# Optimization experiments

Hardware: AMD Instinct MI355X
Metric: run time of the kernel (lower is better)

## Reference

```python
import jax, jax.numpy as jnp
import numpy as np

NUM_ITERATIONS = 3
NUM_ROUTES = 6912  # 32*6*6*6


def _squash(t):
    # t: [..., O]; squash along last dim
    sq = jnp.sum(t * t, axis=-1, keepdims=True)
    return sq * t / ((1.0 + sq) * jnp.sqrt(sq))


def setup_inputs() -> dict:
    key = jax.random.key(0)
    k1, k2 = jax.random.split(key)
    B, R, I, C, O = 64, NUM_ROUTES, 8, 10, 16
    x = jax.random.normal(k1, (B, R, I), dtype=jnp.float32)
    route_weights = jax.random.normal(k2, (C, R, I, O), dtype=jnp.float32)
    return {"x": x, "route_weights": route_weights}


def reference(x, route_weights):
    # x: [B, R, I]; route_weights: [C, R, I, O]
    # priors = x[None,:,:,None,:] @ W[:,None,:,:,:] -> [C, B, R, 1, O]
    priors = jnp.einsum('bri,crio->cbro', x, route_weights)[:, :, :, None, :]
    logits = jnp.zeros_like(priors)  # [C, B, R, 1, O]
    outputs = None
    for i in range(NUM_ITERATIONS):
        # softmax over routes (dim=2), matching custom softmax(input, dim=2)
        probs = jax.nn.softmax(logits, axis=2)
        outputs = _squash(jnp.sum(probs * priors, axis=2, keepdims=True))  # [C,B,1,1,O]
        if i != NUM_ROUTES - 1:  # always true in original (num_routes >> iters)
            delta = jnp.sum(priors * outputs, axis=-1, keepdims=True)  # [C,B,R,1,1]
            logits = logits + delta
    return outputs
```

## Files before the change

kernel.cpp:

```cpp
#include <hip/hip_runtime.h>
#include <math.h>

#define BB 64
#define RR 6912
#define II 8
#define CC 10
#define OO 16
#define RPB2 96
#define NCH2 72
#define NG2 12
#define NBLK 720
#define NREP 9
#define MRG_PAD 20
#define WTILE_I4 (RPB2*16)
#define MRGF (4*64*MRG_PAD + 4*64)
#define ACCW (CC*NREP*BB*OO)
#define ZW   (CC*NREP*BB)
#define BARI (64 + NCH2*32 + NCH2*32)
#define ZWORDS (3*ACCW + 2*ZW + BARI)

typedef _Float16 h2 __attribute__((ext_vector_type(2)));
typedef _Float16 half8 __attribute__((ext_vector_type(8)));
typedef float f32x16 __attribute__((ext_vector_type(16)));
union HV { int4 v; h2 h[4]; half8 h8; };

__device__ __forceinline__ void addf(float* p, float v) {
    float old = __hip_atomic_fetch_add(p, v, __ATOMIC_RELAXED, __HIP_MEMORY_SCOPE_AGENT);
    asm volatile("" :: "v"(old));
}
__device__ __forceinline__ void addi(int* p) {
    int old = __hip_atomic_fetch_add(p, 1, __ATOMIC_RELAXED, __HIP_MEMORY_SCOPE_AGENT);
    asm volatile("" :: "v"(old));
}
__device__ __forceinline__ void xchi(int* p, int v) {
    int old = __hip_atomic_exchange(p, v, __ATOMIC_RELAXED, __HIP_MEMORY_SCOPE_AGENT);
    asm volatile("" :: "v"(old));
}
template <int SLP, int GUARD>
__device__ __forceinline__ void pollge(const int* p, int tgt) {
    int v = __hip_atomic_load(p, __ATOMIC_RELAXED, __HIP_MEMORY_SCOPE_AGENT);
    int g = 0;
    while (v < tgt && ++g < GUARD) {
        __builtin_amdgcn_s_sleep(SLP);
        v = __hip_atomic_load(p, __ATOMIC_RELAXED, __HIP_MEMORY_SCOPE_AGENT);
    }
}

__device__ __forceinline__ void gbar(int* bar, int chunk, int c, int phase) {
    __syncthreads();
    if (threadIdx.x == 0) {
        int* charr = bar + 64 + chunk * 32;
        int* chep  = bar + 64 + NCH2 * 32 + chunk * 32;
        addi(charr);
        if (c == 0) {
            pollge<4, (1 << 14)>(charr, 10 * phase);
            addi(bar + 0);
            if (chunk == 0) {
                pollge<8, (1 << 14)>(bar + 0, NCH2 * phase);
                xchi(bar + 32, phase);
            } else {
                pollge<32, (1 << 12)>(bar + 32, phase);
            }
            xchi(chep, phase);
        } else {
            pollge<8, (1 << 13)>(chep, phase);
        }
    }
    __syncthreads();
}

__global__ __launch_bounds__(256) void prep_kernel(
    const float* __restrict__ x, int4* __restrict__ xth4,
    const float4* __restrict__ w4, int4* __restrict__ wh4,
    float* __restrict__ zbase)
{
    __shared__ __align__(16) float4 lds4[64 * 34];
    const int t = threadIdx.x;
    const int bid = blockIdx.x;

    for (unsigned idx = (unsigned)bid * 256u + (unsigned)t; idx < (unsigned)ZWORDS;
         idx += 1512u * 256u)
        zbase[idx] = 0.f;

    if (bid < 432) {
        const int rblk = bid >> 2;
        const int bblk = bid & 3;
        const int r0 = rblk * 64, b0 = bblk * 16;
        {
            const int rl = t & 63;
            const int bl0 = t >> 6;
#pragma unroll
            for (int kb = 0; kb < 4; ++kb) {
                const int bl = kb * 4 + bl0;
                const float4* src = (const float4*)(x + ((size_t)(b0 + bl) * RR + (r0 + rl)) * II);
                lds4[rl * 34 + bl * 2 + 0] = src[0];
                lds4[rl * 34 + bl * 2 + 1] = src[1];
            }
        }
        __syncthreads();
        {
            const int bl = t & 15;
            const int rw0 = t >> 4;
#pragma unroll
            for (int kr = 0; kr < 4; ++kr) {
                const int rw = kr * 16 + rw0;
                float4 a = lds4[rw * 34 + bl * 2 + 0];
                float4 bq = lds4[rw * 34 + bl * 2 + 1];
                HV u;
                u.h[0] = h2{(_Float16)a.x,  (_Float16)a.y};
                u.h[1] = h2{(_Float16)a.z,  (_Float16)a.w};
                u.h[2] = h2{(_Float16)bq.x, (_Float16)bq.y};
                u.h[3] = h2{(_Float16)bq.z, (_Float16)bq.w};
                xth4[(size_t)(r0 + rw) * BB + (b0 + bl)] = u.v;
            }
        }
    } else {
        _Float16* wl = (_Float16*)lds4;
        const int wblk = bid - 432;
        const int rp = t >> 5;
        const int i  = (t >> 2) & 7;
        const int o0 = (t & 3) * 4;
#pragma unroll 1
        for (int sb = 0; sb < 8; ++sb) {
            const int blk8 = wblk * 8 + sb;
            const float4 v = w4[(size_t)blk8 * 256 + t];
            _Float16* wb = wl + (sb & 1) * 1024;
            wb[(rp * 16 + o0 + 0) * 8 + i] = (_Float16)v.x;
            wb[(rp * 16 + o0 + 1) * 8 + i] = (_Float16)v.y;
            wb[(rp * 16 + o0 + 2) * 8 + i] = (_Float16)v.z;
            wb[(rp * 16 + o0 + 3) * 8 + i] = (_Float16)v.w;
            __syncthreads();
            if (t < 128) wh4[(size_t)blk8 * 128 + t] = ((const int4*)wb)[t];
        }
    }
}

template <int MODE>
__device__ __forceinline__ void it_phase(
    const int4* __restrict__ xth4, const int4* wlds, float* mrg,
    const float* __restrict__ ov,
    float* __restrict__ acc, float* __restrict__ zacc,
    int c, int chunk, int t)
{
    const int wv = t >> 6;
    const int l = t & 63;
    const int b = l & 31;
    const int hi = l >> 5;
    const int aquad = (l >> 4) & 1;
    const bool aact = (aquad == hi);

    float accA[8], accB[8];
#pragma unroll
    for (int j = 0; j < 8; ++j) { accA[j] = 0.f; accB[j] = 0.f; }
    float ZA = 0.f, ZB = 0.f;

    float ovA[8], ovB[8];
    if (MODE != 0) {
        const float* pa = ov + ((size_t)c * BB + b) * OO + 4 * hi;
        const float* pb = ov + ((size_t)c * BB + 32 + b) * OO + 4 * hi;
        float4 a0 = *(const float4*)(pa);
        float4 a1 = *(const float4*)(pa + 8);
        float4 b0 = *(const float4*)(pb);
        float4 b1 = *(const float4*)(pb + 8);
        ovA[0]=a0.x; ovA[1]=a0.y; ovA[2]=a0.z; ovA[3]=a0.w;
        ovA[4]=a1.x; ovA[5]=a1.y; ovA[6]=a1.z; ovA[7]=a1.w;
        ovB[0]=b0.x; ovB[1]=b0.y; ovB[2]=b0.z; ovB[3]=b0.w;
        ovB[4]=b1.x; ovB[5]=b1.y; ovB[6]=b1.z; ovB[7]=b1.w;
    }

    const int rbase = chunk * RPB2 + wv * 24;

    f32x16 cA, cB, zf;
#pragma unroll
    for (int q = 0; q < 16; ++q) { cA[q] = 0.f; cB[q] = 0.f; zf[q] = 0.f; }

    HV xc0, xc1, xn0, xn1;
    xc0.v = xth4[(size_t)(rbase + hi) * BB + b];
    xc1.v = xth4[(size_t)(rbase + hi) * BB + 32 + b];
    xn0 = xc0; xn1 = xc1;

#pragma unroll 1
    for (int g = 0; g < NG2; ++g) {
        if (g + 1 < NG2) {
            const int rn = rbase + (g + 1) * 2 + hi;
            xn0.v = xth4[(size_t)rn * BB + b];
            xn1.v = xth4[(size_t)rn * BB + 32 + b];
        }
        const int rl0 = wv * 24 + g * 2;
        HV wq;
        wq.v = wlds[(rl0 + aquad) * 16 + (l & 15)];
        if (!aact) wq.v = make_int4(0, 0, 0, 0);

        if (MODE == 0) {
            cA = __builtin_amdgcn_mfma_f32_32x32x16_f16(wq.h8, xc0.h8, cA, 0, 0, 0);
            cB = __builtin_amdgcn_mfma_f32_32x32x16_f16(wq.h8, xc1.h8, cB, 0, 0, 0);
        } else {
            f32x16 p0 = __builtin_amdgcn_mfma_f32_32x32x16_f16(wq.h8, xc0.h8, zf, 0, 0, 0);
            f32x16 p1 = __builtin_amdgcn_mfma_f32_32x32x16_f16(wq.h8, xc1.h8, zf, 0, 0, 0);
            float dA0 = 0.f, dA1 = 0.f, dB0 = 0.f, dB1 = 0.f;
#pragma unroll
            for (int j = 0; j < 8; ++j) {
                dA0 = fmaf(p0[j],     ovA[j], dA0);
                dA1 = fmaf(p0[j + 8], ovA[j], dA1);
                dB0 = fmaf(p1[j],     ovB[j], dB0);
                dB1 = fmaf(p1[j + 8], ovB[j], dB1);
            }
            dA0 += __shfl_xor(dA0, 32);
            dA1 += __shfl_xor(dA1, 32);
            dB0 += __shfl_xor(dB0, 32);
            dB1 += __shfl_xor(dB1, 32);
            const float eA0 = __expf(dA0), eA1 = __expf(dA1);
            const float eB0 = __expf(dB0), eB1 = __expf(dB1);
            ZA += eA0 + eA1; ZB += eB0 + eB1;
#pragma unroll
            for (int j = 0; j < 8; ++j) {
                accA[j] = fmaf(eA0, p0[j], fmaf(eA1, p0[j + 8], accA[j]));
                accB[j] = fmaf(eB0, p1[j], fmaf(eB1, p1[j + 8], accB[j]));
            }
        }
        xc0 = xn0; xc1 = xn1;
    }

    if (MODE == 0) {
#pragma unroll
        for (int j = 0; j < 8; ++j) {
            accA[j] = cA[j] + cA[j + 8];
            accB[j] = cB[j] + cB[j + 8];
        }
    }

    {
        float* m0 = mrg + (wv * 64 + b) * MRG_PAD + 4 * hi;
        *(float4*)(m0)     = make_float4(accA[0], accA[1], accA[2], accA[3]);
        *(float4*)(m0 + 8) = make_float4(accA[4], accA[5], accA[6], accA[7]);
        float* m1 = mrg + (wv * 64 + 32 + b) * MRG_PAD + 4 * hi;
        *(float4*)(m1)     = make_float4(accB[0], accB[1], accB[2], accB[3]);
        *(float4*)(m1 + 8) = make_float4(accB[4], accB[5], accB[6], accB[7]);
        if (MODE != 0 && hi == 0) {
            float* zr = mrg + 4 * 64 * MRG_PAD;
            zr[wv * 64 + b] = ZA;
            zr[wv * 64 + 32 + b] = ZB;
        }
    }
    __syncthreads();

    {
        const int b2 = t >> 2, q = t & 3;
        float4 sum = make_float4(0.f, 0.f, 0.f, 0.f);
#pragma unroll
        for (int w2 = 0; w2 < 4; ++w2) {
            const float4 v = *(const float4*)(mrg + (w2 * 64 + b2) * MRG_PAD + q * 4);
            sum.x += v.x; sum.y += v.y; sum.z += v.z; sum.w += v.w;
        }
        const int rep = chunk % NREP;
        float* dst = acc + (((size_t)c * NREP + rep) * BB + b2) * OO + q * 4;
        addf(dst + 0, sum.x);
        addf(dst + 1, sum.y);
        addf(dst + 2, sum.z);
        addf(dst + 3, sum.w);
        if (MODE != 0 && q == 0) {
            const float* zr = mrg + 4 * 64 * MRG_PAD;
            float z = 0.f;
#pragma unroll
            for (int w2 = 0; w2 < 4; ++w2) z += zr[w2 * 64 + b2];
            addf(zacc + ((size_t)c * NREP + rep) * BB + b2, z);
        }
    }
}

template <int MODE>
__device__ __forceinline__ void combine_phase(
    const float* __restrict__ acc, const float* __restrict__ zacc,
    const float* __restrict__ addv, float* __restrict__ dst, bool coh,
    int bid, int t, float* cl)
{
    const int c2 = bid >> 6, b2 = bid & 63;
    const int o = t & 15, g = t >> 4;

    float s = (g < NREP) ? acc[(((size_t)c2 * NREP + g) * BB + b2) * OO + o] : 0.f;
    cl[t] = s;
    if (MODE != 0 && o == 0)
        cl[256 + g] = (g < NREP) ? zacc[((size_t)c2 * NREP + g) * BB + b2] : 0.f;
    __syncthreads();

    if (g == 0) {
#pragma unroll
        for (int k = 1; k < NREP; ++k) s += cl[k * 16 + o];
        if (MODE != 0) {
            float Zt = 0.f;
#pragma unroll
            for (int k = 0; k < NREP; ++k) Zt += cl[256 + k];
            s /= Zt;
        } else {
            s *= (1.0f / RR);
        }
        float sq = s * s;
#pragma unroll
        for (int w = 1; w < 16; w <<= 1) sq += __shfl_xor(sq, w);
        float val = s * sqrtf(sq) / (1.f + sq);
        if (MODE == 1) val += addv[(size_t)bid * OO + o];
        if (coh) {
            float old = __hip_atomic_exchange(dst + (size_t)bid * OO + o, val,
                         __ATOMIC_RELAXED, __HIP_MEMORY_SCOPE_AGENT);
            asm volatile("" :: "v"(old));
        } else {
            dst[(size_t)bid * OO + o] = val;
        }
    }
    __syncthreads();
}

__global__ __launch_bounds__(256, 3) void fused_kernel(
    const int4* __restrict__ xth4, const int4* __restrict__ wh4,
    float* acc0, float* acc1, float* acc2, float* z1, float* z2,
    float* v0, float* outsum, float* out, int* bar)
{
    __shared__ __align__(16) int4 wlds[WTILE_I4];
    __shared__ __align__(16) float mrg[MRGF];
    __shared__ float cl[272];

    const int bid = blockIdx.x;
    const int t = threadIdx.x;
    const int u = (bid & 7) * 90 + (bid >> 3);
    const int chunk = u / 10;
    const int c = u - chunk * 10;

    {
        const int4* src = wh4 + ((size_t)c * RR + (size_t)chunk * RPB2) * 16;
#pragma unroll
        for (int k = 0; k < 6; ++k) wlds[k * 256 + t] = src[k * 256 + t];
    }
    __syncthreads();

    it_phase<0>(xth4, wlds, mrg, nullptr, acc0, nullptr, c, chunk, t);
    gbar(bar, chunk, c, 1);
    if (bid < CC * BB) combine_phase<0>(acc0, nullptr, nullptr, v0, true, bid, t, cl);
    gbar(bar, chunk, c, 2);
    it_phase<1>(xth4, wlds, mrg, v0, acc1, z1, c, chunk, t);
    gbar(bar, chunk, c, 3);
    if (bid < CC * BB) combine_phase<1>(acc1, z1, v0, outsum, true, bid, t, cl);
    gbar(bar, chunk, c, 4);
    it_phase<2>(xth4, wlds, mrg, outsum, acc2, z2, c, chunk, t);
    gbar(bar, chunk, c, 5);
    if (bid < CC * BB) combine_phase<2>(acc2, z2, nullptr, out, false, bid, t, cl);
}

extern "C" void kernel_launch(void* const* d_in, const int* in_sizes, int n_in,
                              void* d_out, int out_size, void* d_ws, size_t ws_size,
                              hipStream_t stream)
{
    const float* x = (const float*)d_in[0];
    const float* w = (const float*)d_in[1];
    float* out = (float*)d_out;

    float* ws = (float*)d_ws;
    float* xth    = ws;
    float* wh     = xth + (size_t)RR * BB * 4;
    float* zbase  = wh + (size_t)CC * RR * 64;
    float* acc0   = zbase;
    float* acc1   = acc0 + ACCW;
    float* acc2   = acc1 + ACCW;
    float* z1     = acc2 + ACCW;
    float* z2     = z1 + ZW;
    int*   bar    = (int*)(z2 + ZW);
    float* v0     = zbase + ZWORDS;
    float* outsum = v0 + CC * BB * OO;

    int4* xth4 = (int4*)xth;
    int4* wh4  = (int4*)wh;
    const float4* w4 = (const float4*)w;

    prep_kernel<<<dim3(432 + 1080), dim3(256), 0, stream>>>(x, xth4, w4, wh4, zbase);
    fused_kernel<<<dim3(NBLK), dim3(256), 0, stream>>>(
        xth4, wh4, acc0, acc1, acc2, z1, z2, v0, outsum, out, bar);
}
```

Measured before the change: 155.5 us.

## Replace global barriers with per-capsule dataflow flags and per-chunk partial buffers

```diff
diff --git a/kernel.cpp b/kernel.cpp
--- a/kernel.cpp
+++ b/kernel.cpp
@@ -10,27 +10,35 @@
 #define NCH2 72
 #define NG2 12
 #define NBLK 720
-#define NREP 9
 #define MRG_PAD 20
 #define WTILE_I4 (RPB2*16)
 #define MRGF (4*64*MRG_PAD + 4*64)
-#define ACCW (CC*NREP*BB*OO)
-#define ZW   (CC*NREP*BB)
-#define BARI (64 + NCH2*32 + NCH2*32)
-#define ZWORDS (3*ACCW + 2*ZW + BARI)
+#define PWW (CC*NCH2*BB*OO)
+#define PZW (CC*NCH2*BB)
+#define L_ARR(c)      ((c) * 32)
+#define L_ARREP(c,r)  ((10 + (c)*8 + (r)) * 32)
+#define L_CD(c)       ((90 + (c)) * 32)
+#define L_RD(c,r)     ((100 + (c)*8 + (r)) * 32)
+#define FLAGI (180*32)
 
 typedef _Float16 h2 __attribute__((ext_vector_type(2)));
 typedef _Float16 half8 __attribute__((ext_vector_type(8)));
 typedef float f32x16 __attribute__((ext_vector_type(16)));
 union HV { int4 v; h2 h[4]; half8 h8; };
 
-__device__ __forceinline__ void addf(float* p, float v) {
-    float old = __hip_atomic_fetch_add(p, v, __ATOMIC_RELAXED, __HIP_MEMORY_SCOPE_AGENT);
+__device__ __forceinline__ void xchf(float* p, float v) {
+    float old = __hip_atomic_exchange(p, v, __ATOMIC_RELAXED, __HIP_MEMORY_SCOPE_AGENT);
     asm volatile("" :: "v"(old));
 }
-__device__ __forceinline__ void addi(int* p) {
-    int old = __hip_atomic_fetch_add(p, 1, __ATOMIC_RELAXED, __HIP_MEMORY_SCOPE_AGENT);
+__device__ __forceinline__ void xchf2(float* p, float a, float b) {
+    union { unsigned long long u; float f[2]; } v;
+    v.f[0] = a; v.f[1] = b;
+    unsigned long long old = __hip_atomic_exchange((unsigned long long*)p, v.u,
+                              __ATOMIC_RELAXED, __HIP_MEMORY_SCOPE_AGENT);
     asm volatile("" :: "v"(old));
+}
+__device__ __forceinline__ int addi(int* p) {
+    return __hip_atomic_fetch_add(p, 1, __ATOMIC_RELAXED, __HIP_MEMORY_SCOPE_AGENT);
 }
 __device__ __forceinline__ void xchi(int* p, int v) {
     int old = __hip_atomic_exchange(p, v, __ATOMIC_RELAXED, __HIP_MEMORY_SCOPE_AGENT);
@@ -46,41 +54,19 @@
     }
 }
 
-__device__ __forceinline__ void gbar(int* bar, int chunk, int c, int phase) {
-    __syncthreads();
-    if (threadIdx.x == 0) {
-        int* charr = bar + 64 + chunk * 32;
-        int* chep  = bar + 64 + NCH2 * 32 + chunk * 32;
-        addi(charr);
-        if (c == 0) {
-            pollge<4, (1 << 14)>(charr, 10 * phase);
-            addi(bar + 0);
-            if (chunk == 0) {
-                pollge<8, (1 << 14)>(bar + 0, NCH2 * phase);
-                xchi(bar + 32, phase);
-            } else {
-                pollge<32, (1 << 12)>(bar + 32, phase);
-            }
-            xchi(chep, phase);
-        } else {
-            pollge<8, (1 << 13)>(chep, phase);
-        }
-    }
-    __syncthreads();
-}
-
 __global__ __launch_bounds__(256) void prep_kernel(
     const float* __restrict__ x, int4* __restrict__ xth4,
     const float4* __restrict__ w4, int4* __restrict__ wh4,
-    float* __restrict__ zbase)
+    int* __restrict__ flags)
 {
     __shared__ __align__(16) float4 lds4[64 * 34];
     const int t = threadIdx.x;
     const int bid = blockIdx.x;
 
-    for (unsigned idx = (unsigned)bid * 256u + (unsigned)t; idx < (unsigned)ZWORDS;
-         idx += 1512u * 256u)
-        zbase[idx] = 0.f;
+    {
+        const unsigned idx = (unsigned)bid * 256u + (unsigned)t;
+        if (idx < (unsigned)FLAGI) flags[idx] = 0;
+    }
 
     if (bid < 432) {
         const int rblk = bid >> 2;
@@ -139,8 +125,8 @@
 __device__ __forceinline__ void it_phase(
     const int4* __restrict__ xth4, const int4* wlds, float* mrg,
     const float* __restrict__ ov,
-    float* __restrict__ acc, float* __restrict__ zacc,
-    int c, int chunk, int t)
+    float* __restrict__ pw, float* __restrict__ pz,
+    int* flags, int c, int chunk, int xcd, int t, int ph)
 {
     const int wv = t >> 6;
     const int l = t & 63;
@@ -148,6 +134,11 @@
     const int hi = l >> 5;
     const int aquad = (l >> 4) & 1;
     const bool aact = (aquad == hi);
+
+    if (MODE != 0) {
+        if (t == 0) pollge<8, (1 << 14)>(flags + L_RD(c, xcd), ph - 1);
+        __syncthreads();
+    }
 
     float accA[8], accB[8];
 #pragma unroll
@@ -252,44 +243,62 @@
             const float4 v = *(const float4*)(mrg + (w2 * 64 + b2) * MRG_PAD + q * 4);
             sum.x += v.x; sum.y += v.y; sum.z += v.z; sum.w += v.w;
         }
-        const int rep = chunk % NREP;
-        float* dst = acc + (((size_t)c * NREP + rep) * BB + b2) * OO + q * 4;
-        addf(dst + 0, sum.x);
-        addf(dst + 1, sum.y);
-        addf(dst + 2, sum.z);
-        addf(dst + 3, sum.w);
+        float* dst = pw + (((size_t)(c * NCH2 + chunk) * BB + b2) * OO) + q * 4;
+        xchf2(dst + 0, sum.x, sum.y);
+        xchf2(dst + 2, sum.z, sum.w);
         if (MODE != 0 && q == 0) {
             const float* zr = mrg + 4 * 64 * MRG_PAD;
             float z = 0.f;
 #pragma unroll
             for (int w2 = 0; w2 < 4; ++w2) z += zr[w2 * 64 + b2];
-            addf(zacc + ((size_t)c * NREP + rep) * BB + b2, z);
+            xchf(pz + (size_t)(c * NCH2 + chunk) * BB + b2, z);
+        }
+    }
+
+    __syncthreads();
+    if (t == 0) {
+        const int old = addi(flags + L_ARR(c));
+        if (old == NCH2 * ph - 1) {
+#pragma unroll
+            for (int r = 0; r < 8; ++r) xchi(flags + L_ARREP(c, r), ph);
         }
     }
 }
 
 template <int MODE>
 __device__ __forceinline__ void combine_phase(
-    const float* __restrict__ acc, const float* __restrict__ zacc,
+    const float* __restrict__ pw, const float* __restrict__ pzw,
     const float* __restrict__ addv, float* __restrict__ dst, bool coh,
-    int bid, int t, float* cl)
+    int* flags, int bid, int t, float* cl, int ph)
 {
     const int c2 = bid >> 6, b2 = bid & 63;
     const int o = t & 15, g = t >> 4;
 
-    float s = (g < NREP) ? acc[(((size_t)c2 * NREP + g) * BB + b2) * OO + o] : 0.f;
+    if (t == 0) pollge<8, (1 << 14)>(flags + L_ARREP(c2, bid & 7), ph);
+    __syncthreads();
+
+    const float* base = pw + (size_t)c2 * NCH2 * (BB * OO);
+    float s = 0.f, zl = 0.f;
+#pragma unroll
+    for (int k = 0; k < 5; ++k) {
+        const int rid = g + k * 16;
+        if (rid < NCH2) {
+            s += base[(size_t)rid * (BB * OO) + b2 * OO + o];
+            if (MODE != 0 && o == 0)
+                zl += pzw[(size_t)c2 * NCH2 * BB + (size_t)rid * BB + b2];
+        }
+    }
     cl[t] = s;
-    if (MODE != 0 && o == 0)
-        cl[256 + g] = (g < NREP) ? zacc[((size_t)c2 * NREP + g) * BB + b2] : 0.f;
+    if (MODE != 0 && o == 0) cl[256 + g] = zl;
     __syncthreads();
 
     if (g == 0) {
 #pragma unroll
-        for (int k = 1; k < NREP; ++k) s += cl[k * 16 + o];
+        for (int k = 1; k < 16; ++k) s += cl[k * 16 + o];
         if (MODE != 0) {
             float Zt = 0.f;
 #pragma unroll
-            for (int k = 0; k < NREP; ++k) Zt += cl[256 + k];
+            for (int k = 0; k < 16; ++k) Zt += cl[256 + k];
             s /= Zt;
         } else {
             s *= (1.0f / RR);
@@ -299,21 +308,24 @@
         for (int w = 1; w < 16; w <<= 1) sq += __shfl_xor(sq, w);
         float val = s * sqrtf(sq) / (1.f + sq);
         if (MODE == 1) val += addv[(size_t)bid * OO + o];
-        if (coh) {
-            float old = __hip_atomic_exchange(dst + (size_t)bid * OO + o, val,
-                         __ATOMIC_RELAXED, __HIP_MEMORY_SCOPE_AGENT);
-            asm volatile("" :: "v"(old));
-        } else {
-            dst[(size_t)bid * OO + o] = val;
-        }
-    }
-    __syncthreads();
+        if (coh) xchf(dst + (size_t)bid * OO + o, val);
+        else     dst[(size_t)bid * OO + o] = val;
+    }
+    __syncthreads();
+
+    if (MODE != 2 && t == 0) {
+        const int old = addi(flags + L_CD(c2));
+        if (old == CC * BB / CC * ph - 1) {
+#pragma unroll
+            for (int r = 0; r < 8; ++r) xchi(flags + L_RD(c2, r), ph);
+        }
+    }
 }
 
 __global__ __launch_bounds__(256, 3) void fused_kernel(
     const int4* __restrict__ xth4, const int4* __restrict__ wh4,
-    float* acc0, float* acc1, float* acc2, float* z1, float* z2,
-    float* v0, float* outsum, float* out, int* bar)
+    float* pw0, float* pw1, float* pw2, float* pz1, float* pz2,
+    float* v0, float* outsum, float* out, int* flags)
 {
     __shared__ __align__(16) int4 wlds[WTILE_I4];
     __shared__ __align__(16) float mrg[MRGF];
@@ -321,7 +333,8 @@
 
     const int bid = blockIdx.x;
     const int t = threadIdx.x;
-    const int u = (bid & 7) * 90 + (bid >> 3);
+    const int xcd = bid & 7;
+    const int u = xcd * 90 + (bid >> 3);
     const int chunk = u / 10;
     const int c = u - chunk * 10;
 
@@ -332,17 +345,12 @@
     }
     __syncthreads();
 
-    it_phase<0>(xth4, wlds, mrg, nullptr, acc0, nullptr, c, chunk, t);
-    gbar(bar, chunk, c, 1);
-    if (bid < CC * BB) combine_phase<0>(acc0, nullptr, nullptr, v0, true, bid, t, cl);
-    gbar(bar, chunk, c, 2);
-    it_phase<1>(xth4, wlds, mrg, v0, acc1, z1, c, chunk, t);
-    gbar(bar, chunk, c, 3);
-    if (bid < CC * BB) combine_phase<1>(acc1, z1, v0, outsum, true, bid, t, cl);
-    gbar(bar, chunk, c, 4);
-    it_phase<2>(xth4, wlds, mrg, outsum, acc2, z2, c, chunk, t);
-    gbar(bar, chunk, c, 5);
-    if (bid < CC * BB) combine_phase<2>(acc2, z2, nullptr, out, false, bid, t, cl);
+    it_phase<0>(xth4, wlds, mrg, nullptr, pw0, nullptr, flags, c, chunk, xcd, t, 1);
+    if (bid < CC * BB) combine_phase<0>(pw0, nullptr, nullptr, v0, true, flags, bid, t, cl, 1);
+    it_phase<1>(xth4, wlds, mrg, v0, pw1, pz1, flags, c, chunk, xcd, t, 2);
+    if (bid < CC * BB) combine_phase<1>(pw1, pz1, v0, outsum, true, flags, bid, t, cl, 2);
+    it_phase<2>(xth4, wlds, mrg, outsum, pw2, pz2, flags, c, chunk, xcd, t, 3);
+    if (bid < CC * BB) combine_phase<2>(pw2, pz2, nullptr, out, false, flags, bid, t, cl, 3);
 }
 
 extern "C" void kernel_launch(void* const* d_in, const int* in_sizes, int n_in,
@@ -356,21 +364,20 @@
     float* ws = (float*)d_ws;
     float* xth    = ws;
     float* wh     = xth + (size_t)RR * BB * 4;
-    float* zbase  = wh + (size_t)CC * RR * 64;
-    float* acc0   = zbase;
-    float* acc1   = acc0 + ACCW;
-    float* acc2   = acc1 + ACCW;
-    float* z1     = acc2 + ACCW;
-    float* z2     = z1 + ZW;
-    int*   bar    = (int*)(z2 + ZW);
-    float* v0     = zbase + ZWORDS;
+    float* pw0    = wh + (size_t)CC * RR * 64;
+    float* pw1    = pw0 + PWW;
+    float* pw2    = pw1 + PWW;
+    float* pz1    = pw2 + PWW;
+    float* pz2    = pz1 + PZW;
+    float* v0     = pz2 + PZW;
     float* outsum = v0 + CC * BB * OO;
+    int*   flags  = (int*)(outsum + CC * BB * OO);
 
     int4* xth4 = (int4*)xth;
     int4* wh4  = (int4*)wh;
     const float4* w4 = (const float4*)w;
 
-    prep_kernel<<<dim3(432 + 1080), dim3(256), 0, stream>>>(x, xth4, w4, wh4, zbase);
+    prep_kernel<<<dim3(432 + 1080), dim3(256), 0, stream>>>(x, xth4, w4, wh4, flags);
     fused_kernel<<<dim3(NBLK), dim3(256), 0, stream>>>(
-        xth4, wh4, acc0, acc1, acc2, z1, z2, v0, outsum, out, bar);
-}
+        xth4, wh4, pw0, pw1, pw2, pz1, pz2, v0, outsum, out, flags);
+}
```

After: 141.6 us. -8.9%, faster.
